# Kernel tuning notes

Measured on AMD Instinct MI355X. Metric: run time of the kernel, lower is better.

Reference implementation:

```python
import jax, jax.numpy as jnp
import numpy as np

IN_C, H, W = 64, 256, 256
K = 3
OUT_C = 128


def setup_inputs() -> dict:
    key = jax.random.key(0)
    k1, k2 = jax.random.split(key)
    x = jax.random.normal(k1, (IN_C, H, W), dtype=jnp.float32)
    limit = np.sqrt(6.0 / (IN_C * K * K + OUT_C)).astype(np.float32)
    kernels = jax.random.uniform(k2, (OUT_C, IN_C, K, K), minval=-limit, maxval=limit, dtype=jnp.float32)
    biases = jnp.zeros((OUT_C,), dtype=jnp.float32)
    return {"x": x, "kernels": kernels, "biases": biases}


def reference(x, kernels, biases):
    # Cross-correlation (patch * kernel, no flip), VALID padding, CHW single image.
    out = jax.lax.conv_general_dilated(
        x[None],                      # [1, C, H, W]
        kernels,                      # [O, I, K, K]
        window_strides=(1, 1),
        padding="VALID",
        dimension_numbers=("NCHW", "OIHW", "NCHW"),
    )[0]                              # [O, H-K+1, W-K+1]
    return out + biases[:, None, None]
```

## Files before the change

kernel.cpp:

```cpp
#include <hip/hip_runtime.h>
#include <stdint.h>

#define IN_C 64
#define HH 256
#define WW 256
#define HW (HH * WW)
#define OUT_C 128
#define OH 254
#define OW 254
#define OHW (OH * OW)

#define XR 6
#define XW 66
#define CPAD 72

typedef __attribute__((ext_vector_type(4))) float f32x4;
typedef __attribute__((ext_vector_type(8))) __bf16 bf16x8;

__device__ __forceinline__ unsigned short f2bf(float f) {
  union { float f; unsigned u; } v; v.f = f;
  unsigned r = v.u + 0x7FFFu + ((v.u >> 16) & 1u);
  return (unsigned short)(r >> 16);
}

__global__ void prep_w(const float* __restrict__ w, unsigned short* __restrict__ wt) {
  const int idx = blockIdx.x * 256 + threadIdx.x;
  if (idx >= 9 * 8192) return;
  const int j    = idx & 7;
  const int lane = (idx >> 3) & 63;
  const int mt   = (idx >> 9) & 7;
  const int ch   = (idx >> 12) & 1;
  const int tap  = idx >> 13;
  const int o = mt * 16 + (lane & 15);
  const int c = ch * 32 + (lane >> 4) * 8 + j;
  wt[idx] = f2bf(w[(o * IN_C + c) * 9 + tap]);
}

__global__ __launch_bounds__(512, 2) void conv_mfma(
    const float* __restrict__ x, const unsigned short* __restrict__ wt,
    const float* __restrict__ bias, float* __restrict__ out) {
  __shared__ __align__(16) unsigned short Xs[XR * XW * CPAD];

  const int tid  = threadIdx.x;
  const int wave = tid >> 6;
  const int lane = tid & 63;
  const int x0 = blockIdx.x * 64;
  const int y0 = blockIdx.y * 4;

  const int mhalf = wave & 1;
  const int row   = wave >> 1;
  const int nlane = lane & 15;
  const int quad  = lane >> 4;

  const bf16x8* __restrict__ Wp = ((const bf16x8*)wt) + lane + (mhalf * 4) * 64;
  bf16x8 afA[4], afB[4];
#pragma unroll
  for (int mt = 0; mt < 4; ++mt) afA[mt] = Wp[mt * 64];

  {
    const int cq = tid & 15;
    const int xh = (tid >> 4) & 15;
    const int r3 = (tid >> 8) * 3;
#pragma unroll
    for (int k = 0; k < 3; ++k) {
      const int r = r3 + k;
      const int yr = (y0 + r > 255) ? 255 : (y0 + r);
      const float* bx = x + yr * WW + x0 + xh * 4;
      f32x4 vv[4];
#pragma unroll
      for (int cc = 0; cc < 4; ++cc)
        vv[cc] = *(const f32x4*)(bx + (cq * 4 + cc) * HW);
#pragma unroll
      for (int xxi = 0; xxi < 4; ++xxi) {
        unsigned u0 = (unsigned)f2bf(vv[0][xxi]) | ((unsigned)f2bf(vv[1][xxi]) << 16);
        unsigned u1 = (unsigned)f2bf(vv[2][xxi]) | ((unsigned)f2bf(vv[3][xxi]) << 16);
        *(uint2*)&Xs[(r * XW + xh * 4 + xxi) * CPAD + cq * 4] = make_uint2(u0, u1);
      }
    }
    for (int k = tid; k < 768; k += 512) {
      const int c = k & 63;
      const int q = k >> 6;
      const int xxt = 64 + (q & 1);
      const int r = q >> 1;
      const int yr = (y0 + r > 255) ? 255 : (y0 + r);
      int xg = x0 + xxt;
      if (xg > WW - 1) xg = WW - 1;
      Xs[(r * XW + xxt) * CPAD + c] = f2bf(x[c * HW + yr * WW + xg]);
    }
  }

  f32x4 acc[4][4];
#pragma unroll
  for (int mt = 0; mt < 4; ++mt) {
    const f32x4 bv = *(const f32x4*)(bias + (mhalf * 4 + mt) * 16 + quad * 4);
#pragma unroll
    for (int nt = 0; nt < 4; ++nt) acc[mt][nt] = bv;
  }

  __syncthreads();

#pragma unroll 1
  for (int pair = 0; pair < 9; ++pair) {
    const int ky = pair / 3;
    const int kx = pair - ky * 3;
    const int r = row + ky;
    const unsigned short* xrow = &Xs[(r * XW + kx) * CPAD + quad * 8];

#pragma unroll
    for (int mt = 0; mt < 4; ++mt) afB[mt] = Wp[((2 * pair + 1) * 8 + mt) * 64];

    {
      bf16x8 bfr[4];
#pragma unroll
      for (int nt = 0; nt < 4; ++nt)
        bfr[nt] = *(const bf16x8*)&xrow[(nt * 16 + nlane) * CPAD];
#pragma unroll
      for (int mt = 0; mt < 4; ++mt)
#pragma unroll
        for (int nt = 0; nt < 4; ++nt)
          acc[mt][nt] = __builtin_amdgcn_mfma_f32_16x16x32_bf16(afA[mt], bfr[nt], acc[mt][nt], 0, 0, 0);
    }

    if (pair < 8) {
#pragma unroll
      for (int mt = 0; mt < 4; ++mt) afA[mt] = Wp[((2 * pair + 2) * 8 + mt) * 64];
    }

    {
      bf16x8 bfr[4];
#pragma unroll
      for (int nt = 0; nt < 4; ++nt)
        bfr[nt] = *(const bf16x8*)&xrow[(nt * 16 + nlane) * CPAD + 32];
#pragma unroll
      for (int mt = 0; mt < 4; ++mt)
#pragma unroll
        for (int nt = 0; nt < 4; ++nt)
          acc[mt][nt] = __builtin_amdgcn_mfma_f32_16x16x32_bf16(afB[mt], bfr[nt], acc[mt][nt], 0, 0, 0);
    }
  }

  const int y = y0 + row;
  if (y < OH) {
#pragma unroll
    for (int mt = 0; mt < 4; ++mt) {
      const int obase = (mhalf * 4 + mt) * 16 + quad * 4;
#pragma unroll
      for (int nt = 0; nt < 4; ++nt) {
        const int xc = x0 + nt * 16 + nlane;
        if (xc < OW) {
          float* dst = out + obase * OHW + y * OW + xc;
#pragma unroll
          for (int reg = 0; reg < 4; ++reg)
            dst[reg * OHW] = acc[mt][nt][reg];
        }
      }
    }
  }
}

extern "C" void kernel_launch(void* const* d_in, const int* in_sizes, int n_in,
                              void* d_out, int out_size, void* d_ws, size_t ws_size,
                              hipStream_t stream) {
  const float* x = (const float*)d_in[0];
  const float* w = (const float*)d_in[1];
  const float* b = (const float*)d_in[2];
  float* out = (float*)d_out;
  unsigned short* wt = (unsigned short*)d_ws;

  prep_w<<<dim3(288), dim3(256), 0, stream>>>(w, wt);
  conv_mfma<<<dim3(4, 64), dim3(512), 0, stream>>>(x, wt, b, out);
}
```

Before: 87.80 us.

## Halve conv block to two output rows and batch staging loads

Each block now covers two output rows with 256 threads instead of four rows with 512. The grid grows to 127 row-blocks, which removes the out-of-range last-row work and the clamping. The staging code issues all 16 vector loads and the halo loads before doing any bf16 conversion, so more memory loads are in flight at once. Overlapping input rows are now loaded by more blocks, and the larger number of loaded values raises register pressure.

```diff
diff --git a/kernel.cpp b/kernel.cpp
--- a/kernel.cpp
+++ b/kernel.cpp
@@ -10,7 +10,7 @@
 #define OW 254
 #define OHW (OH * OW)
 
-#define XR 6
+#define XR 4
 #define XW 66
 #define CPAD 72
 
@@ -36,7 +36,7 @@
   wt[idx] = f2bf(w[(o * IN_C + c) * 9 + tap]);
 }
 
-__global__ __launch_bounds__(512, 2) void conv_mfma(
+__global__ __launch_bounds__(256, 3) void conv_mfma(
     const float* __restrict__ x, const unsigned short* __restrict__ wt,
     const float* __restrict__ bias, float* __restrict__ out) {
   __shared__ __align__(16) unsigned short Xs[XR * XW * CPAD];
@@ -45,7 +45,7 @@
   const int wave = tid >> 6;
   const int lane = tid & 63;
   const int x0 = blockIdx.x * 64;
-  const int y0 = blockIdx.y * 4;
+  const int y0 = blockIdx.y * 2;
 
   const int mhalf = wave & 1;
   const int row   = wave >> 1;
@@ -59,34 +59,43 @@
 
   {
     const int cq = tid & 15;
-    const int xh = (tid >> 4) & 15;
-    const int r3 = (tid >> 8) * 3;
+    const int xh = tid >> 4;
+
+    int hc[2], hr[2], hx[2];
+    float hv[2];
 #pragma unroll
-    for (int k = 0; k < 3; ++k) {
-      const int r = r3 + k;
-      const int yr = (y0 + r > 255) ? 255 : (y0 + r);
-      const float* bx = x + yr * WW + x0 + xh * 4;
-      f32x4 vv[4];
+    for (int h = 0; h < 2; ++h) {
+      const int k = tid + h * 256;
+      hc[h] = k & 63;
+      const int q = k >> 6;
+      hx[h] = 64 + (q & 1);
+      hr[h] = q >> 1;
+      int xg = x0 + hx[h];
+      if (xg > WW - 1) xg = WW - 1;
+      hv[h] = x[hc[h] * HW + (y0 + hr[h]) * WW + xg];
+    }
+
+    f32x4 vv[4][4];
+#pragma unroll
+    for (int r = 0; r < 4; ++r) {
+      const float* bx = x + (y0 + r) * WW + x0 + xh * 4;
 #pragma unroll
       for (int cc = 0; cc < 4; ++cc)
-        vv[cc] = *(const f32x4*)(bx + (cq * 4 + cc) * HW);
+        vv[r][cc] = *(const f32x4*)(bx + (cq * 4 + cc) * HW);
+    }
+
+#pragma unroll
+    for (int r = 0; r < 4; ++r) {
 #pragma unroll
       for (int xxi = 0; xxi < 4; ++xxi) {
-        unsigned u0 = (unsigned)f2bf(vv[0][xxi]) | ((unsigned)f2bf(vv[1][xxi]) << 16);
-        unsigned u1 = (unsigned)f2bf(vv[2][xxi]) | ((unsigned)f2bf(vv[3][xxi]) << 16);
+        unsigned u0 = (unsigned)f2bf(vv[r][0][xxi]) | ((unsigned)f2bf(vv[r][1][xxi]) << 16);
+        unsigned u1 = (unsigned)f2bf(vv[r][2][xxi]) | ((unsigned)f2bf(vv[r][3][xxi]) << 16);
         *(uint2*)&Xs[(r * XW + xh * 4 + xxi) * CPAD + cq * 4] = make_uint2(u0, u1);
       }
     }
-    for (int k = tid; k < 768; k += 512) {
-      const int c = k & 63;
-      const int q = k >> 6;
-      const int xxt = 64 + (q & 1);
-      const int r = q >> 1;
-      const int yr = (y0 + r > 255) ? 255 : (y0 + r);
-      int xg = x0 + xxt;
-      if (xg > WW - 1) xg = WW - 1;
-      Xs[(r * XW + xxt) * CPAD + c] = f2bf(x[c * HW + yr * WW + xg]);
-    }
+#pragma unroll
+    for (int h = 0; h < 2; ++h)
+      Xs[(hr[h] * XW + hx[h]) * CPAD + hc[h]] = f2bf(hv[h]);
   }
 
   f32x4 acc[4][4];
@@ -140,19 +149,17 @@
   }
 
   const int y = y0 + row;
-  if (y < OH) {
 #pragma unroll
-    for (int mt = 0; mt < 4; ++mt) {
-      const int obase = (mhalf * 4 + mt) * 16 + quad * 4;
+  for (int mt = 0; mt < 4; ++mt) {
+    const int obase = (mhalf * 4 + mt) * 16 + quad * 4;
 #pragma unroll
-      for (int nt = 0; nt < 4; ++nt) {
-        const int xc = x0 + nt * 16 + nlane;
-        if (xc < OW) {
-          float* dst = out + obase * OHW + y * OW + xc;
+    for (int nt = 0; nt < 4; ++nt) {
+      const int xc = x0 + nt * 16 + nlane;
+      if (xc < OW) {
+        float* dst = out + obase * OHW + y * OW + xc;
 #pragma unroll
-          for (int reg = 0; reg < 4; ++reg)
-            dst[reg * OHW] = acc[mt][nt][reg];
-        }
+        for (int reg = 0; reg < 4; ++reg)
+          dst[reg * OHW] = acc[mt][nt][reg];
       }
     }
   }
@@ -168,5 +175,5 @@
   unsigned short* wt = (unsigned short*)d_ws;
 
   prep_w<<<dim3(288), dim3(256), 0, stream>>>(w, wt);
-  conv_mfma<<<dim3(4, 64), dim3(512), 0, stream>>>(x, wt, b, out);
+  conv_mfma<<<dim3(4, 127), dim3(256), 0, stream>>>(x, wt, b, out);
 }
```

Measured after the change: 91.54 us. 4.3% more time.
